# Kernel tuning notes

Hardware: AMD Instinct MI355X
Metric: run time of the kernel (lower is better)

Reference implementation:

```python
import jax, jax.numpy as jnp
import numpy as np

OUT_F, IN_F, BLOCK, RANK = 8192, 8192, 32, 16
B, S = 4, 256
Q_ZERO = 128.0      # symmetric int8-style zero point for the Q8_0-like quants
LORA_SCALE = 2.0    # patch alpha applied by the patch function


def setup_inputs() -> dict:
    key = jax.random.key(0)
    k1, k2, k3, k4, k5, k6 = jax.random.split(key, 6)
    x = jax.random.normal(k1, (B, S, IN_F), dtype=jnp.float32)
    # block-quantized weight: int quants in [0,256) and per-block scales
    q_int = jax.random.randint(k2, (OUT_F, IN_F // BLOCK, BLOCK), 0, 256, dtype=jnp.int32)
    scales = jax.random.uniform(k3, (OUT_F, IN_F // BLOCK), dtype=jnp.float32) * 0.02
    lora_A = jax.random.normal(k4, (RANK, IN_F), dtype=jnp.float32) * 0.02
    lora_B = jax.random.normal(k5, (OUT_F, RANK), dtype=jnp.float32) * 0.02
    bias = jax.random.normal(k6, (OUT_F,), dtype=jnp.float32)
    return {"x": x, "q_int": q_int, "scales": scales,
            "lora_A": lora_A, "lora_B": lora_B, "bias": bias}


def reference(x, q_int, scales, lora_A, lora_B, bias):
    # --- get_weight(): dequantize GGML block-quantized tensor ---
    # w[o, b, e] = (q[o, b, e] - 128) * scale[o, b]
    w = (q_int.astype(jnp.float32) - Q_ZERO) * scales[:, :, None]   # [out, in//BLOCK, BLOCK]
    w = w.reshape(OUT_F, IN_F)                                      # [out, in]
    # --- apply patch function (LoRA add) ---
    w = w + LORA_SCALE * (lora_B @ lora_A)                          # [out, in]
    # --- cast_bias_weight + F.linear ---
    w = w.astype(x.dtype)
    y = jnp.einsum('bsi,oi->bso', x, w) + bias.astype(x.dtype)      # [B, S, out]
    return y
```

## Files before the change

### kernel.cpp

```cpp
#include <hip/hip_runtime.h>
#include <hip/hip_bf16.h>
#include <stdint.h>

#define OUT_F 8192
#define IN_F  8192
#define RANK  16
#define M_TOT 1024
#define BM 128
#define BN 64
#define BK 64
#define WP 72
#define NK (IN_F / BK)

typedef __bf16 bf16x8 __attribute__((ext_vector_type(8)));
typedef float  f32x4  __attribute__((ext_vector_type(4)));

static __device__ __forceinline__ uint32_t pack_bf16(float lo, float hi) {
    uint32_t a = __builtin_bit_cast(uint32_t, lo);
    uint32_t b = __builtin_bit_cast(uint32_t, hi);
    return ((a + 0x8000u) >> 16) | ((b + 0x8000u) & 0xffff0000u);
}

__global__ __launch_bounds__(256) void convert_kernel(
    const float* __restrict__ x, uint2* __restrict__ xb2, float* __restrict__ t)
{
    const int tid = threadIdx.x, b = blockIdx.x;
    if (b < 64) t[b * 256 + tid] = 0.f;
    const float4* x4 = (const float4*)x;
    const int base = b * 256 + tid;
#pragma unroll
    for (int j = 0; j < 8; ++j) {
        const int i = base + j * 262144;
        const float4 v = x4[i];
        uint2 p;
        p.x = pack_bf16(v.x, v.y);
        p.y = pack_bf16(v.z, v.w);
        xb2[i] = p;
    }
}

__global__ __launch_bounds__(256) void lora_t_kernel(
    const float* __restrict__ x, const float* __restrict__ lora_A,
    float* __restrict__ t)
{
    const int b = blockIdx.x;
    const int mt = b >> 4, ks = b & 15;
    const int tid = threadIdx.x, wave = tid >> 6, lane = tid & 63;
    const int fr = lane & 15, quad = lane >> 4;
    const int m = mt * 64 + wave * 16 + fr;
    const int k0 = ks * 512 + quad * 8;

    f32x4 acc = {0.f, 0.f, 0.f, 0.f};
    const float* xr = x + (size_t)m * IN_F + k0;
    const float* ar = lora_A + (size_t)fr * IN_F + k0;

#pragma unroll 4
    for (int s = 0; s < 16; ++s) {
        const float4 x0 = *(const float4*)(xr + s * 32);
        const float4 x1 = *(const float4*)(xr + s * 32 + 4);
        const float4 a0 = *(const float4*)(ar + s * 32);
        const float4 a1 = *(const float4*)(ar + s * 32 + 4);
        bf16x8 af, bfr;
        uint32_t* ap = (uint32_t*)&af;
        uint32_t* bp = (uint32_t*)&bfr;
        ap[0] = pack_bf16(x0.x, x0.y); ap[1] = pack_bf16(x0.z, x0.w);
        ap[2] = pack_bf16(x1.x, x1.y); ap[3] = pack_bf16(x1.z, x1.w);
        bp[0] = pack_bf16(a0.x, a0.y); bp[1] = pack_bf16(a0.z, a0.w);
        bp[2] = pack_bf16(a1.x, a1.y); bp[3] = pack_bf16(a1.z, a1.w);
        acc = __builtin_amdgcn_mfma_f32_16x16x32_bf16(af, bfr, acc, 0, 0, 0);
    }
    const int mout = mt * 64 + wave * 16 + quad * 4;
#pragma unroll
    for (int r = 0; r < 4; ++r)
        atomicAdd(&t[(size_t)(mout + r) * RANK + fr], acc[r]);
}

__global__ __launch_bounds__(256, 4) void gemm_kernel(
    const uint16_t* __restrict__ xb,
    const int*      __restrict__ q,
    const float*    __restrict__ scales,
    const float*    __restrict__ t,
    const float*    __restrict__ loraB,
    const float*    __restrict__ bias,
    float*          __restrict__ out)
{
    __shared__ __align__(16) uint16_t xs[BM * BK];
    __shared__ __align__(16) uint16_t wt[BN * WP];

    const int bx    = blockIdx.x;
    const int mtile = bx >> 7;
    const int ntile = bx & 127;
    const int m0 = mtile * BM;
    const int n0 = ntile * BN;

    const int tid  = threadIdx.x;
    const int wave = tid >> 6;
    const int lane = tid & 63;
    const int wm = wave & 1, wn = wave >> 1;
    const int fr = lane & 15;
    const int quad = lane >> 4;
    const int fk = quad * 8;

    const int qrow  = tid >> 4;
    const int qcol4 = (tid & 15) * 4;
    const int qhi   = (tid >> 3) & 1;

    f32x4 acc[4][2];
    const f32x4 z = {0.f, 0.f, 0.f, 0.f};
#pragma unroll
    for (int i = 0; i < 4; ++i)
#pragma unroll
        for (int j = 0; j < 2; ++j) acc[i][j] = z;

    const int* qbase = q + (size_t)n0 * IN_F + qcol4;
    int4  qv[4];
    float sc[4];
#pragma unroll
    for (int j = 0; j < 4; ++j) {
        const int row = qrow + 16 * j;
        qv[j] = *(const int4*)(qbase + (size_t)row * IN_F);
        sc[j] = scales[(size_t)(n0 + row) * (IN_F / 32) + qhi];
    }

    {
        if (tid < 128) {
            const int row = tid;
            const int s = row & 7;
            const float4* tp = (const float4*)(t + (size_t)(m0 + row) * RANK);
            const float4 v0 = tp[0], v1 = tp[1], v2 = tp[2], v3 = tp[3];
            uint32_t vals[8];
            vals[0] = pack_bf16(v0.x, v0.y); vals[1] = pack_bf16(v0.z, v0.w);
            vals[2] = pack_bf16(v1.x, v1.y); vals[3] = pack_bf16(v1.z, v1.w);
            vals[4] = pack_bf16(v2.x, v2.y); vals[5] = pack_bf16(v2.z, v2.w);
            vals[6] = pack_bf16(v3.x, v3.y); vals[7] = pack_bf16(v3.z, v3.w);
            uint32_t* dst = (uint32_t*)(xs + row * BK);
#pragma unroll
            for (int c = 0; c < 8; ++c) {
                const int p = (c ^ s) * 4;
                if (c < 2) {
                    dst[p + 0] = vals[c * 4 + 0]; dst[p + 1] = vals[c * 4 + 1];
                    dst[p + 2] = vals[c * 4 + 2]; dst[p + 3] = vals[c * 4 + 3];
                } else {
                    dst[p + 0] = 0; dst[p + 1] = 0; dst[p + 2] = 0; dst[p + 3] = 0;
                }
            }
        } else if (tid < 192) {
            const int row = tid - 128;
            const float4* bp = (const float4*)(loraB + (size_t)(n0 + row) * RANK);
            const float4 v0 = bp[0], v1 = bp[1], v2 = bp[2], v3 = bp[3];
            uint32_t* dst = (uint32_t*)(wt + row * WP);
            dst[0] = pack_bf16(2.f * v0.x, 2.f * v0.y); dst[1] = pack_bf16(2.f * v0.z, 2.f * v0.w);
            dst[2] = pack_bf16(2.f * v1.x, 2.f * v1.y); dst[3] = pack_bf16(2.f * v1.z, 2.f * v1.w);
            dst[4] = pack_bf16(2.f * v2.x, 2.f * v2.y); dst[5] = pack_bf16(2.f * v2.z, 2.f * v2.w);
            dst[6] = pack_bf16(2.f * v3.x, 2.f * v3.y); dst[7] = pack_bf16(2.f * v3.z, 2.f * v3.w);
#pragma unroll
            for (int i = 8; i < 16; ++i) dst[i] = 0;
        }
        __syncthreads();
        bf16x8 af[4], bfr[2];
#pragma unroll
        for (int i = 0; i < 4; ++i) {
            const int R = wm * 64 + i * 16 + fr;
            const int p = (quad ^ (fr & 7)) * 8;
            af[i] = *(const bf16x8*)(xs + R * BK + p);
        }
#pragma unroll
        for (int j = 0; j < 2; ++j)
            bfr[j] = *(const bf16x8*)(wt + (wn * 32 + j * 16 + fr) * WP + fk);
#pragma unroll
        for (int i = 0; i < 4; ++i)
#pragma unroll
            for (int j = 0; j < 2; ++j)
                acc[i][j] = __builtin_amdgcn_mfma_f32_16x16x32_bf16(af[i], bfr[j], acc[i][j], 0, 0, 0);
    }

    const int xrow   = wave * 32 + (lane >> 3);
    const int xchunk = (lane & 7) ^ (lane >> 3);
    const uint16_t* xsrc = xb + (size_t)(m0 + xrow) * IN_F + xchunk * 8;

    for (int kt = 0; kt < NK; ++kt) {
        __syncthreads();

#pragma unroll
        for (int i = 0; i < 4; ++i) {
            __builtin_amdgcn_global_load_lds(
                (const __attribute__((address_space(1))) uint32_t*)(xsrc + kt * BK + (size_t)i * 8 * IN_F),
                (__attribute__((address_space(3))) uint32_t*)(xs + (wave * 32 + i * 8) * BK),
                16, 0, 0);
        }
#pragma unroll
        for (int j = 0; j < 4; ++j) {
            const float s = sc[j];
            const float c = -128.f * s;
            const float f0 = fmaf((float)qv[j].x, s, c);
            const float f1 = fmaf((float)qv[j].y, s, c);
            const float f2 = fmaf((float)qv[j].z, s, c);
            const float f3 = fmaf((float)qv[j].w, s, c);
            uint2 p;
            p.x = pack_bf16(f0, f1);
            p.y = pack_bf16(f2, f3);
            *(uint2*)(wt + (qrow + 16 * j) * WP + qcol4) = p;
        }
        __syncthreads();

        {
            const int ktn = (kt + 1) & (NK - 1);
#pragma unroll
            for (int j = 0; j < 4; ++j) {
                const int row = qrow + 16 * j;
                qv[j] = *(const int4*)(qbase + (size_t)row * IN_F + ktn * BK);
                sc[j] = scales[(size_t)(n0 + row) * (IN_F / 32) + ktn * 2 + qhi];
            }
        }

#pragma unroll
        for (int kk = 0; kk < BK; kk += 32) {
            bf16x8 af[4], bfr[2];
#pragma unroll
            for (int i = 0; i < 4; ++i) {
                const int R = wm * 64 + i * 16 + fr;
                const int p = (((kk >> 3) + quad) ^ (fr & 7)) * 8;
                af[i] = *(const bf16x8*)(xs + R * BK + p);
            }
#pragma unroll
            for (int j = 0; j < 2; ++j)
                bfr[j] = *(const bf16x8*)(wt + (wn * 32 + j * 16 + fr) * WP + kk + fk);
#pragma unroll
            for (int i = 0; i < 4; ++i)
#pragma unroll
                for (int j = 0; j < 2; ++j)
                    acc[i][j] = __builtin_amdgcn_mfma_f32_16x16x32_bf16(af[i], bfr[j], acc[i][j], 0, 0, 0);
        }
    }

#pragma unroll
    for (int j = 0; j < 2; ++j) {
        const int col = n0 + wn * 32 + j * 16 + fr;
        const float bv = bias[col];
#pragma unroll
        for (int i = 0; i < 4; ++i) {
            const int rbase = m0 + wm * 64 + i * 16 + quad * 4;
#pragma unroll
            for (int r = 0; r < 4; ++r)
                out[(size_t)(rbase + r) * OUT_F + col] = acc[i][j][r] + bv;
        }
    }
}

extern "C" void kernel_launch(void* const* d_in, const int* in_sizes, int n_in,
                              void* d_out, int out_size, void* d_ws, size_t ws_size,
                              hipStream_t stream) {
    const float* x      = (const float*)d_in[0];
    const int*   q      = (const int*)d_in[1];
    const float* scales = (const float*)d_in[2];
    const float* lora_A = (const float*)d_in[3];
    const float* lora_B = (const float*)d_in[4];
    const float* bias   = (const float*)d_in[5];
    float* out = (float*)d_out;

    uint16_t* xb = (uint16_t*)d_ws;
    float*    t  = (float*)((char*)d_ws + (size_t)M_TOT * IN_F * sizeof(uint16_t));

    convert_kernel<<<M_TOT, 256, 0, stream>>>(x, (uint2*)xb, t);
    lora_t_kernel<<<256, 256, 0, stream>>>(x, lora_A, t);
    gemm_kernel<<<(M_TOT / BM) * (OUT_F / BN), 256, 0, stream>>>(
        xb, q, scales, t, lora_B, bias, out);
}
```

Before: 624.6 us.

## Double-buffer LDS tiles, widen N tile to 128, prefetch quants two steps ahead

```diff
diff --git a/kernel.cpp b/kernel.cpp
--- a/kernel.cpp
+++ b/kernel.cpp
@@ -7,10 +7,10 @@
 #define RANK  16
 #define M_TOT 1024
 #define BM 128
-#define BN 64
+#define BN 128
 #define BK 64
-#define WP 72
 #define NK (IN_F / BK)
+#define SCB (IN_F / 32)
 
 typedef __bf16 bf16x8 __attribute__((ext_vector_type(8)));
 typedef float  f32x4  __attribute__((ext_vector_type(4)));
@@ -75,7 +75,54 @@
         atomicAdd(&t[(size_t)(mout + r) * RANK + fr], acc[r]);
 }
 
-__global__ __launch_bounds__(256, 4) void gemm_kernel(
+
+#define GEMM_STEP(KT, P, CUR, NXT)                                             \
+    {                                                                          \
+        const int ktn = ((KT) + 2) & (NK - 1);                                 \
+        _Pragma("unroll")                                                      \
+        for (int j = 0; j < 8; ++j) {                                          \
+            const int row = qrow + 16 * j;                                     \
+            qv[(P) ^ 1][j] = *(const int4*)(qbase + (size_t)row * IN_F + ktn * BK); \
+            sc[(P) ^ 1][j] = scales[(size_t)(n0 + row) * SCB + ktn * 2 + qhi]; \
+        }                                                                      \
+        const int kta = ((KT) + 1) & (NK - 1);                                 \
+        _Pragma("unroll")                                                      \
+        for (int i = 0; i < 4; ++i) {                                          \
+            __builtin_amdgcn_global_load_lds(                                  \
+                (const __attribute__((address_space(1))) uint32_t*)(xsrc + (size_t)kta * BK + (size_t)i * 8 * IN_F), \
+                (__attribute__((address_space(3))) uint32_t*)(&xs[NXT][(wave * 32 + i * 8) * BK]), \
+                16, 0, 0);                                                     \
+        }                                                                      \
+        _Pragma("unroll")                                                      \
+        for (int j = 0; j < 8; ++j) {                                          \
+            const float s = sc[P][j];                                          \
+            const float c = -128.f * s;                                        \
+            const int4 qq = qv[P][j];                                          \
+            uint2 pk;                                                          \
+            pk.x = pack_bf16(fmaf((float)qq.x, s, c), fmaf((float)qq.y, s, c)); \
+            pk.y = pack_bf16(fmaf((float)qq.z, s, c), fmaf((float)qq.w, s, c)); \
+            *(uint2*)(&wt[NXT][(qrow + 16 * j) * BK + wpos]) = pk;             \
+        }                                                                      \
+        _Pragma("unroll")                                                      \
+        for (int kk = 0; kk < BK; kk += 32) {                                  \
+            bf16x8 af[4], bfr[4];                                              \
+            const int pp = (((kk >> 3) + quad) ^ (fr & 7)) * 8;                \
+            _Pragma("unroll")                                                  \
+            for (int i = 0; i < 4; ++i)                                        \
+                af[i] = *(const bf16x8*)(&xs[CUR][(wm * 64 + i * 16 + fr) * BK + pp]); \
+            _Pragma("unroll")                                                  \
+            for (int j = 0; j < 4; ++j)                                        \
+                bfr[j] = *(const bf16x8*)(&wt[CUR][(wn * 64 + j * 16 + fr) * BK + pp]); \
+            _Pragma("unroll")                                                  \
+            for (int i = 0; i < 4; ++i)                                        \
+                _Pragma("unroll")                                              \
+                for (int j = 0; j < 4; ++j)                                    \
+                    acc[i][j] = __builtin_amdgcn_mfma_f32_16x16x32_bf16(af[i], bfr[j], acc[i][j], 0, 0, 0); \
+        }                                                                      \
+        __syncthreads();                                                       \
+    }
+
+__global__ __launch_bounds__(256, 2) void gemm_kernel(
     const uint16_t* __restrict__ xb,
     const int*      __restrict__ q,
     const float*    __restrict__ scales,
@@ -84,12 +131,12 @@
     const float*    __restrict__ bias,
     float*          __restrict__ out)
 {
-    __shared__ __align__(16) uint16_t xs[BM * BK];
-    __shared__ __align__(16) uint16_t wt[BN * WP];
+    __shared__ __align__(16) uint16_t xs[2][BM * BK];
+    __shared__ __align__(16) uint16_t wt[2][BN * BK];
 
     const int bx    = blockIdx.x;
-    const int mtile = bx >> 7;
-    const int ntile = bx & 127;
+    const int mtile = bx >> 6;
+    const int ntile = bx & 63;
     const int m0 = mtile * BM;
     const int n0 = ntile * BN;
 
@@ -99,33 +146,34 @@
     const int wm = wave & 1, wn = wave >> 1;
     const int fr = lane & 15;
     const int quad = lane >> 4;
-    const int fk = quad * 8;
 
     const int qrow  = tid >> 4;
     const int qcol4 = (tid & 15) * 4;
     const int qhi   = (tid >> 3) & 1;
-
-    f32x4 acc[4][2];
+    const int wpos = ((((tid >> 1) & 7) ^ (qrow & 7)) * 8) + (tid & 1) * 4;
+
+    const int* qbase = q + (size_t)n0 * IN_F + qcol4;
+
+    f32x4 acc[4][4];
     const f32x4 z = {0.f, 0.f, 0.f, 0.f};
 #pragma unroll
     for (int i = 0; i < 4; ++i)
 #pragma unroll
-        for (int j = 0; j < 2; ++j) acc[i][j] = z;
-
-    const int* qbase = q + (size_t)n0 * IN_F + qcol4;
-    int4  qv[4];
-    float sc[4];
-#pragma unroll
-    for (int j = 0; j < 4; ++j) {
+        for (int j = 0; j < 4; ++j) acc[i][j] = z;
+
+    int4  qv[2][8];
+    float sc[2][8];
+
+#pragma unroll
+    for (int j = 0; j < 8; ++j) {
         const int row = qrow + 16 * j;
-        qv[j] = *(const int4*)(qbase + (size_t)row * IN_F);
-        sc[j] = scales[(size_t)(n0 + row) * (IN_F / 32) + qhi];
+        qv[0][j] = *(const int4*)(qbase + (size_t)row * IN_F);
+        sc[0][j] = scales[(size_t)(n0 + row) * SCB + qhi];
     }
 
     {
         if (tid < 128) {
-            const int row = tid;
-            const int s = row & 7;
+            const int row = tid, s = row & 7;
             const float4* tp = (const float4*)(t + (size_t)(m0 + row) * RANK);
             const float4 v0 = tp[0], v1 = tp[1], v2 = tp[2], v3 = tp[3];
             uint32_t vals[8];
@@ -133,7 +181,7 @@
             vals[2] = pack_bf16(v1.x, v1.y); vals[3] = pack_bf16(v1.z, v1.w);
             vals[4] = pack_bf16(v2.x, v2.y); vals[5] = pack_bf16(v2.z, v2.w);
             vals[6] = pack_bf16(v3.x, v3.y); vals[7] = pack_bf16(v3.z, v3.w);
-            uint32_t* dst = (uint32_t*)(xs + row * BK);
+            uint32_t* dst = (uint32_t*)(&xs[0][row * BK]);
 #pragma unroll
             for (int c = 0; c < 8; ++c) {
                 const int p = (c ^ s) * 4;
@@ -144,98 +192,81 @@
                     dst[p + 0] = 0; dst[p + 1] = 0; dst[p + 2] = 0; dst[p + 3] = 0;
                 }
             }
-        } else if (tid < 192) {
-            const int row = tid - 128;
+        } else {
+            const int row = tid - 128, s = row & 7;
             const float4* bp = (const float4*)(loraB + (size_t)(n0 + row) * RANK);
             const float4 v0 = bp[0], v1 = bp[1], v2 = bp[2], v3 = bp[3];
-            uint32_t* dst = (uint32_t*)(wt + row * WP);
-            dst[0] = pack_bf16(2.f * v0.x, 2.f * v0.y); dst[1] = pack_bf16(2.f * v0.z, 2.f * v0.w);
-            dst[2] = pack_bf16(2.f * v1.x, 2.f * v1.y); dst[3] = pack_bf16(2.f * v1.z, 2.f * v1.w);
-            dst[4] = pack_bf16(2.f * v2.x, 2.f * v2.y); dst[5] = pack_bf16(2.f * v2.z, 2.f * v2.w);
-            dst[6] = pack_bf16(2.f * v3.x, 2.f * v3.y); dst[7] = pack_bf16(2.f * v3.z, 2.f * v3.w);
-#pragma unroll
-            for (int i = 8; i < 16; ++i) dst[i] = 0;
+            uint32_t vals[8];
+            vals[0] = pack_bf16(2.f * v0.x, 2.f * v0.y); vals[1] = pack_bf16(2.f * v0.z, 2.f * v0.w);
+            vals[2] = pack_bf16(2.f * v1.x, 2.f * v1.y); vals[3] = pack_bf16(2.f * v1.z, 2.f * v1.w);
+            vals[4] = pack_bf16(2.f * v2.x, 2.f * v2.y); vals[5] = pack_bf16(2.f * v2.z, 2.f * v2.w);
+            vals[6] = pack_bf16(2.f * v3.x, 2.f * v3.y); vals[7] = pack_bf16(2.f * v3.z, 2.f * v3.w);
+            uint32_t* dst = (uint32_t*)(&wt[0][row * BK]);
+#pragma unroll
+            for (int c = 0; c < 8; ++c) {
+                const int p = (c ^ s) * 4;
+                if (c < 2) {
+                    dst[p + 0] = vals[c * 4 + 0]; dst[p + 1] = vals[c * 4 + 1];
+                    dst[p + 2] = vals[c * 4 + 2]; dst[p + 3] = vals[c * 4 + 3];
+                } else {
+                    dst[p + 0] = 0; dst[p + 1] = 0; dst[p + 2] = 0; dst[p + 3] = 0;
+                }
+            }
         }
         __syncthreads();
-        bf16x8 af[4], bfr[2];
-#pragma unroll
-        for (int i = 0; i < 4; ++i) {
-            const int R = wm * 64 + i * 16 + fr;
-            const int p = (quad ^ (fr & 7)) * 8;
-            af[i] = *(const bf16x8*)(xs + R * BK + p);
-        }
-#pragma unroll
-        for (int j = 0; j < 2; ++j)
-            bfr[j] = *(const bf16x8*)(wt + (wn * 32 + j * 16 + fr) * WP + fk);
+        const int pp = (quad ^ (fr & 7)) * 8;
+        bf16x8 af[4], bfr[4];
 #pragma unroll
         for (int i = 0; i < 4; ++i)
-#pragma unroll
-            for (int j = 0; j < 2; ++j)
+            af[i] = *(const bf16x8*)(&xs[0][(wm * 64 + i * 16 + fr) * BK + pp]);
+#pragma unroll
+        for (int j = 0; j < 4; ++j)
+            bfr[j] = *(const bf16x8*)(&wt[0][(wn * 64 + j * 16 + fr) * BK + pp]);
+#pragma unroll
+        for (int i = 0; i < 4; ++i)
+#pragma unroll
+            for (int j = 0; j < 4; ++j)
                 acc[i][j] = __builtin_amdgcn_mfma_f32_16x16x32_bf16(af[i], bfr[j], acc[i][j], 0, 0, 0);
+        __syncthreads();
     }
 
     const int xrow   = wave * 32 + (lane >> 3);
     const int xchunk = (lane & 7) ^ (lane >> 3);
     const uint16_t* xsrc = xb + (size_t)(m0 + xrow) * IN_F + xchunk * 8;
 
-    for (int kt = 0; kt < NK; ++kt) {
-        __syncthreads();
-
-#pragma unroll
-        for (int i = 0; i < 4; ++i) {
-            __builtin_amdgcn_global_load_lds(
-                (const __attribute__((address_space(1))) uint32_t*)(xsrc + kt * BK + (size_t)i * 8 * IN_F),
-                (__attribute__((address_space(3))) uint32_t*)(xs + (wave * 32 + i * 8) * BK),
-                16, 0, 0);
-        }
-#pragma unroll
-        for (int j = 0; j < 4; ++j) {
-            const float s = sc[j];
-            const float c = -128.f * s;
-            const float f0 = fmaf((float)qv[j].x, s, c);
-            const float f1 = fmaf((float)qv[j].y, s, c);
-            const float f2 = fmaf((float)qv[j].z, s, c);
-            const float f3 = fmaf((float)qv[j].w, s, c);
-            uint2 p;
-            p.x = pack_bf16(f0, f1);
-            p.y = pack_bf16(f2, f3);
-            *(uint2*)(wt + (qrow + 16 * j) * WP + qcol4) = p;
-        }
-        __syncthreads();
-
-        {
-            const int ktn = (kt + 1) & (NK - 1);
-#pragma unroll
-            for (int j = 0; j < 4; ++j) {
-                const int row = qrow + 16 * j;
-                qv[j] = *(const int4*)(qbase + (size_t)row * IN_F + ktn * BK);
-                sc[j] = scales[(size_t)(n0 + row) * (IN_F / 32) + ktn * 2 + qhi];
-            }
-        }
-
-#pragma unroll
-        for (int kk = 0; kk < BK; kk += 32) {
-            bf16x8 af[4], bfr[2];
-#pragma unroll
-            for (int i = 0; i < 4; ++i) {
-                const int R = wm * 64 + i * 16 + fr;
-                const int p = (((kk >> 3) + quad) ^ (fr & 7)) * 8;
-                af[i] = *(const bf16x8*)(xs + R * BK + p);
-            }
-#pragma unroll
-            for (int j = 0; j < 2; ++j)
-                bfr[j] = *(const bf16x8*)(wt + (wn * 32 + j * 16 + fr) * WP + kk + fk);
-#pragma unroll
-            for (int i = 0; i < 4; ++i)
-#pragma unroll
-                for (int j = 0; j < 2; ++j)
-                    acc[i][j] = __builtin_amdgcn_mfma_f32_16x16x32_bf16(af[i], bfr[j], acc[i][j], 0, 0, 0);
-        }
-    }
-
-#pragma unroll
-    for (int j = 0; j < 2; ++j) {
-        const int col = n0 + wn * 32 + j * 16 + fr;
+#pragma unroll
+    for (int i = 0; i < 4; ++i) {
+        __builtin_amdgcn_global_load_lds(
+            (const __attribute__((address_space(1))) uint32_t*)(xsrc + (size_t)i * 8 * IN_F),
+            (__attribute__((address_space(3))) uint32_t*)(&xs[0][(wave * 32 + i * 8) * BK]),
+            16, 0, 0);
+    }
+#pragma unroll
+    for (int j = 0; j < 8; ++j) {
+        const float s = sc[0][j];
+        const float c = -128.f * s;
+        const int4 qq = qv[0][j];
+        uint2 pk;
+        pk.x = pack_bf16(fmaf((float)qq.x, s, c), fmaf((float)qq.y, s, c));
+        pk.y = pack_bf16(fmaf((float)qq.z, s, c), fmaf((float)qq.w, s, c));
+        *(uint2*)(&wt[0][(qrow + 16 * j) * BK + wpos]) = pk;
+    }
+#pragma unroll
+    for (int j = 0; j < 8; ++j) {
+        const int row = qrow + 16 * j;
+        qv[0][j] = *(const int4*)(qbase + (size_t)row * IN_F + 1 * BK);
+        sc[0][j] = scales[(size_t)(n0 + row) * SCB + 2 + qhi];
+    }
+    __syncthreads();
+
+    for (int kt = 0; kt < NK; kt += 2) {
+        GEMM_STEP(kt,     0, 0, 1);
+        GEMM_STEP(kt + 1, 1, 1, 0);
+    }
+
+#pragma unroll
+    for (int j = 0; j < 4; ++j) {
+        const int col = n0 + wn * 64 + j * 16 + fr;
         const float bv = bias[col];
 #pragma unroll
         for (int i = 0; i < 4; ++i) {
```

New measurement: 606.6 us. 1.03x faster.
